# Optimization experiments

Measured on AMD Instinct MI355X. Metric: run time of the kernel, lower is better.

## Reference

```python
import jax, jax.numpy as jnp
import numpy as np

B, D, H, R, OUT = 16384, 1024, 4, 1024, 10
LN_EPS = 1e-5


def setup_inputs() -> dict:
    key = jax.random.key(0)
    ks = jax.random.split(key, 20)
    s_in = 1.0 / np.sqrt(D)
    s_hid = 1.0 / np.sqrt(H * R)
    inp = {
        'x': jax.random.normal(ks[0], (B, D), dtype=jnp.float32),
        # block 1
        'wr1': jax.random.normal(ks[1], (H, R, D), dtype=jnp.float32) * s_in,
        'br1': jnp.zeros((H, R), dtype=jnp.float32),
        'wl1': jax.random.normal(ks[2], (H, R, D), dtype=jnp.float32) * s_in,
        'bl1': jnp.zeros((H, R), dtype=jnp.float32),
        'we1': jax.random.normal(ks[3], (D, H * R), dtype=jnp.float32) * s_hid,
        'be1': jnp.zeros((D,), dtype=jnp.float32),
        'g1': jnp.ones((D,), dtype=jnp.float32),
        'b1': jnp.zeros((D,), dtype=jnp.float32),
        # block 2
        'wr2': jax.random.normal(ks[4], (H, R, D), dtype=jnp.float32) * s_in,
        'br2': jnp.zeros((H, R), dtype=jnp.float32),
        'wl2': jax.random.normal(ks[5], (H, R, D), dtype=jnp.float32) * s_in,
        'bl2': jnp.zeros((H, R), dtype=jnp.float32),
        'we2': jax.random.normal(ks[6], (D, H * R), dtype=jnp.float32) * s_hid,
        'be2': jnp.zeros((D,), dtype=jnp.float32),
        'g2': jnp.ones((D,), dtype=jnp.float32),
        'b2': jnp.zeros((D,), dtype=jnp.float32),
        # final linear
        'wf': jax.random.normal(ks[7], (OUT, D), dtype=jnp.float32) * s_in,
        'bf': jnp.zeros((OUT,), dtype=jnp.float32),
    }
    return inp


def _bilinear_block(x, wr, br, wl, bl, we, be):
    # per-basis right/left projections batched into one einsum each: [B,D] x [H,R,D] -> [B,H,R]
    right = jnp.einsum('bd,hrd->bhr', x, wr) + br
    left = jnp.einsum('bd,hrd->bhr', x, wl) + bl
    # elementwise bilinear interaction, concat bases along last dim -> [B, H*R]
    inter = (right * left).reshape(x.shape[0], -1)
    return inter @ we.T + be  # [B, D_out]


def _layernorm(x, g, b):
    mu = jnp.mean(x, axis=-1, keepdims=True)
    var = jnp.mean(jnp.square(x - mu), axis=-1, keepdims=True)
    return (x - mu) * jax.lax.rsqrt(var + LN_EPS) * g + b


def reference(x, wr1, br1, wl1, bl1, we1, be1, g1, b1,
              wr2, br2, wl2, bl2, we2, be2, g2, b2, wf, bf):
    # block 1: bilinear + residual + layernorm
    h = _layernorm(x + _bilinear_block(x, wr1, br1, wl1, bl1, we1, be1), g1, b1)
    # block 2
    h = _layernorm(h + _bilinear_block(h, wr2, br2, wl2, bl2, we2, be2), g2, b2)
    # final linear head
    return h @ wf.T + bf
```

## Files before the change

### kernel.cpp

```cpp
#include <hip/hip_runtime.h>
#include <hip/hip_fp16.h>

#define DEV static __device__ __forceinline__

typedef _Float16 f16;
typedef _Float16 f16x8 __attribute__((ext_vector_type(8)));
typedef _Float16 f16x4 __attribute__((ext_vector_type(4)));
typedef float f32x4 __attribute__((ext_vector_type(4)));

constexpr int BATCH = 16384;
constexpr int D = 1024;
constexpr int HR = 4096;
constexpr int NOUT = 10;

__global__ void k_conv4(const float* __restrict__ s0, f16* __restrict__ d0, int n0,
                        const float* __restrict__ s1, f16* __restrict__ d1, int n1,
                        const float* __restrict__ s2, f16* __restrict__ d2, int n2,
                        const float* __restrict__ s3, f16* __restrict__ d3, int n3) {
    int i = blockIdx.x * blockDim.x + threadIdx.x;
    const int st = gridDim.x * blockDim.x;
    const int tot = n0 + n1 + n2 + n3;
    for (; i < tot; i += st) {
        const float* s; f16* d; int j = i;
        if (j < n0) { s = s0; d = d0; }
        else {
            j -= n0;
            if (j < n1) { s = s1; d = d1; }
            else {
                j -= n1;
                if (j < n2) { s = s2; d = d2; }
                else { j -= n2; s = s3; d = d3; }
            }
        }
        float4 v = reinterpret_cast<const float4*>(s)[j];
        f16x4 h;
        h[0] = (f16)v.x; h[1] = (f16)v.y; h[2] = (f16)v.z; h[3] = (f16)v.w;
        reinterpret_cast<f16x4*>(d)[j] = h;
    }
}

DEV void stage16(void* lds, const void* g) {
    __builtin_amdgcn_global_load_lds(
        (const __attribute__((address_space(1))) void*)g,
        (__attribute__((address_space(3))) void*)lds,
        16, 0, 0);
}

DEV void xcd_map(int bid, int MT, int& mt, int& nt) {
    const int x = bid & 7, q = bid >> 3;
    const int mpx = MT >> 3;
    nt = q / mpx;
    mt = x * mpx + (q % mpx);
}

#define VMCNT(n) asm volatile("s_waitcnt vmcnt(" #n ")" ::: "memory")
#define BAR()    __builtin_amdgcn_s_barrier()
#define PRIO(p)  __builtin_amdgcn_s_setprio(p)

__global__ __launch_bounds__(512, 2) void k_gemm_dual(
    const f16* __restrict__ Xh, const f16* __restrict__ Wr, const f16* __restrict__ Wl,
    const float* __restrict__ br, const float* __restrict__ bl,
    f16* __restrict__ inter, int MT)
{
    extern __shared__ __align__(16) char smem[];
    constexpr int NT = 16;
    constexpr int BUF = 65536;
    constexpr int OA = 0, OR = 32768, OL = 49152;

    int mt, nt;
    xcd_map(blockIdx.x, MT, mt, nt);
    const int m0 = mt * 256, n0 = nt * 128;
    const int tid = threadIdx.x;
    const int lane = tid & 63, wid = tid >> 6;
    const int wm = wid >> 2, wn = wid & 3;
    const int fr = lane & 15, fq = lane >> 4;
    const int xs = (fr & 7) << 4;
    const int dst = tid * 16;

    const int lr = tid >> 3;
    const int cb = ((tid & 7) << 4) ^ ((lr & 7) << 4);
    const char* pA0 = (const char*)Xh + (size_t)(m0 + lr)       * 2048 + cb;
    const char* pA1 = (const char*)Xh + (size_t)(m0 + 128 + lr) * 2048 + cb;
    const char* pA2 = (const char*)Xh + (size_t)(m0 + 64 + lr)  * 2048 + cb;
    const char* pA3 = (const char*)Xh + (size_t)(m0 + 192 + lr) * 2048 + cb;
    const char* pR0 = (const char*)Wr + (size_t)(n0 + lr)       * 2048 + cb;
    const char* pR1 = (const char*)Wr + (size_t)(n0 + 64 + lr)  * 2048 + cb;
    const char* pL0 = (const char*)Wl + (size_t)(n0 + lr)       * 2048 + cb;
    const char* pL1 = (const char*)Wl + (size_t)(n0 + 64 + lr)  * 2048 + cb;

#define D_AOFF(mi,mf,ks) (OA + ((mi)*128 + wm*64 + (mf)*16 + fr)*128 + ((((ks)*64) + fq*16) ^ xs))
#define D_ROFF(nf,ks)    (OR + (wn*32 + (nf)*16 + fr)*128 + ((((ks)*64) + fq*16) ^ xs))
#define D_LOFF(nf,ks)    (OL + (wn*32 + (nf)*16 + fr)*128 + ((((ks)*64) + fq*16) ^ xs))

    f16x8 a[4][2], bR[2][2], bL[2][2];
    f32x4 accR[8][2] = {};
    f32x4 accL[8][2] = {};

    stage16(smem + OA + dst, pA0);          stage16(smem + OA + 8192 + dst, pA1);
    stage16(smem + OR + dst, pR0);          stage16(smem + OR + 8192 + dst, pR1);
    stage16(smem + OL + dst, pL0);          stage16(smem + OL + 8192 + dst, pL1);
    stage16(smem + OA + 16384 + dst, pA2);  stage16(smem + OA + 24576 + dst, pA3);
    VMCNT(4);
    BAR();

    long ko = 128;
    for (int t = 0; t < NT; ++t) {
        char* base = smem + (t & 1) * BUF;
        char* nb   = smem + ((t & 1) ^ 1) * BUF;
        const bool pf = (t + 1) < NT;

#pragma unroll
        for (int mf = 0; mf < 4; ++mf)
#pragma unroll
            for (int ks = 0; ks < 2; ++ks)
                a[mf][ks] = *(const f16x8*)(base + D_AOFF(0, mf, ks));
#pragma unroll
        for (int nf = 0; nf < 2; ++nf)
#pragma unroll
            for (int ks = 0; ks < 2; ++ks)
                bR[nf][ks] = *(const f16x8*)(base + D_ROFF(nf, ks));
        if (pf) { stage16(nb + OA + dst, pA0 + ko); stage16(nb + OA + 8192 + dst, pA1 + ko); }
        PRIO(1);
#pragma unroll
        for (int mf = 0; mf < 4; ++mf)
#pragma unroll
            for (int nf = 0; nf < 2; ++nf)
#pragma unroll
                for (int ks = 0; ks < 2; ++ks)
                    accR[mf][nf] = __builtin_amdgcn_mfma_f32_16x16x32_f16(a[mf][ks], bR[nf][ks], accR[mf][nf], 0, 0, 0);
        PRIO(0);
        if (pf) { VMCNT(4); } else { VMCNT(2); }
        BAR();

#pragma unroll
        for (int nf = 0; nf < 2; ++nf)
#pragma unroll
            for (int ks = 0; ks < 2; ++ks)
                bL[nf][ks] = *(const f16x8*)(base + D_LOFF(nf, ks));
        if (pf) { stage16(nb + OR + dst, pR0 + ko); stage16(nb + OR + 8192 + dst, pR1 + ko); }
        PRIO(1);
#pragma unroll
        for (int mf = 0; mf < 4; ++mf)
#pragma unroll
            for (int nf = 0; nf < 2; ++nf)
#pragma unroll
                for (int ks = 0; ks < 2; ++ks)
                    accL[mf][nf] = __builtin_amdgcn_mfma_f32_16x16x32_f16(a[mf][ks], bL[nf][ks], accL[mf][nf], 0, 0, 0);
        PRIO(0);
        if (pf) { VMCNT(4); } else { VMCNT(0); }
        BAR();

#pragma unroll
        for (int mf = 0; mf < 4; ++mf)
#pragma unroll
            for (int ks = 0; ks < 2; ++ks)
                a[mf][ks] = *(const f16x8*)(base + D_AOFF(1, mf, ks));
        if (pf) { stage16(nb + OL + dst, pL0 + ko); stage16(nb + OL + 8192 + dst, pL1 + ko); }
        PRIO(1);
#pragma unroll
        for (int mf = 0; mf < 4; ++mf)
#pragma unroll
            for (int nf = 0; nf < 2; ++nf)
#pragma unroll
                for (int ks = 0; ks < 2; ++ks)
                    accR[4 + mf][nf] = __builtin_amdgcn_mfma_f32_16x16x32_f16(a[mf][ks], bR[nf][ks], accR[4 + mf][nf], 0, 0, 0);
        PRIO(0);
        BAR();

        if (pf) { stage16(nb + OA + 16384 + dst, pA2 + ko); stage16(nb + OA + 24576 + dst, pA3 + ko); }
        PRIO(1);
#pragma unroll
        for (int mf = 0; mf < 4; ++mf)
#pragma unroll
            for (int nf = 0; nf < 2; ++nf)
#pragma unroll
                for (int ks = 0; ks < 2; ++ks)
                    accL[4 + mf][nf] = __builtin_amdgcn_mfma_f32_16x16x32_f16(a[mf][ks], bL[nf][ks], accL[4 + mf][nf], 0, 0, 0);
        PRIO(0);
        if (pf) { VMCNT(4); }
        BAR();

        ko += 128;
    }

#pragma unroll
    for (int nf = 0; nf < 2; ++nf) {
        const int gc = n0 + wn * 32 + nf * 16 + fr;
        const float brv = br[gc], blv = bl[gc];
#pragma unroll
        for (int mi = 0; mi < 2; ++mi)
#pragma unroll
            for (int mf = 0; mf < 4; ++mf) {
                const int gr0 = m0 + wm * 128 + mi * 64 + mf * 16 + fq * 4;
#pragma unroll
                for (int j = 0; j < 4; ++j) {
                    const float rv = accR[mi * 4 + mf][nf][j] + brv;
                    const float lv = accL[mi * 4 + mf][nf][j] + blv;
                    inter[(size_t)(gr0 + j) * HR + gc] = (f16)(rv * lv);
                }
            }
    }
#undef D_AOFF
#undef D_ROFF
#undef D_LOFF
}

__global__ __launch_bounds__(512, 2) void k_gemm_expand_f32r(
    const f16* __restrict__ Ain, const f16* __restrict__ Wt,
    const float* __restrict__ be, const float* __restrict__ resid,
    f16* __restrict__ E, int MT);
__global__ __launch_bounds__(512, 2) void k_gemm_expand_f16r(
    const f16* __restrict__ Ain, const f16* __restrict__ Wt,
    const float* __restrict__ be, const f16* __restrict__ resid,
    f16* __restrict__ E, int MT);

template <typename TR>
DEV void expand_body(const f16* Ain, const f16* Wt, const float* be,
                     const TR* resid, f16* E, int MT)
{
    extern __shared__ __align__(16) char smem[];
    constexpr int NT = 64;
    constexpr int BUF = 65536;
    constexpr int OA = 0, OB = 32768;

    int mt, nt;
    xcd_map(blockIdx.x, MT, mt, nt);
    const int m0 = mt * 256, n0 = nt * 256;
    const int tid = threadIdx.x;
    const int lane = tid & 63, wid = tid >> 6;
    const int wm = wid >> 2, wn = wid & 3;
    const int fr = lane & 15, fq = lane >> 4;
    const int xs = (fr & 7) << 4;
    const int dst = tid * 16;

    const int lr = tid >> 3;
    const int cb = ((tid & 7) << 4) ^ ((lr & 7) << 4);
    const char* pA0 = (const char*)Ain + (size_t)(m0 + lr)       * 8192 + cb;
    const char* pA1 = (const char*)Ain + (size_t)(m0 + 128 + lr) * 8192 + cb;
    const char* pA2 = (const char*)Ain + (size_t)(m0 + 64 + lr)  * 8192 + cb;
    const char* pA3 = (const char*)Ain + (size_t)(m0 + 192 + lr) * 8192 + cb;
    const int r5 = lr & 31, wn2 = lr >> 5;
    const char* pB0 = (const char*)Wt + (size_t)(n0 + wn2 * 64 + r5)        * 8192 + cb;
    const char* pB1 = (const char*)Wt + (size_t)(n0 + (2 + wn2) * 64 + r5)  * 8192 + cb;
    const char* pB2 = (const char*)Wt + (size_t)(n0 + wn2 * 64 + 32 + r5)       * 8192 + cb;
    const char* pB3 = (const char*)Wt + (size_t)(n0 + (2 + wn2) * 64 + 32 + r5) * 8192 + cb;

#define E_AOFF(mi,mf,ks) (OA + ((mi)*128 + wm*64 + (mf)*16 + fr)*128 + ((((ks)*64) + fq*16) ^ xs))
#define E_BOFF(ni,nf,ks) (OB + ((ni)*128 + wn*32 + (nf)*16 + fr)*128 + ((((ks)*64) + fq*16) ^ xs))

    f16x8 a[4][2], b0[2][2], b1[2][2];
    f32x4 acc[8][4] = {};

    stage16(smem + OA + dst, pA0);          stage16(smem + OA + 8192 + dst, pA1);
    stage16(smem + OB + dst, pB0);          stage16(smem + OB + 8192 + dst, pB1);
    stage16(smem + OB + 16384 + dst, pB2);  stage16(smem + OB + 24576 + dst, pB3);
    stage16(smem + OA + 16384 + dst, pA2);  stage16(smem + OA + 24576 + dst, pA3);
    VMCNT(4);
    BAR();

    long ko = 128;
    for (int t = 0; t < NT; ++t) {
        char* base = smem + (t & 1) * BUF;
        char* nb   = smem + ((t & 1) ^ 1) * BUF;
        const bool pf = (t + 1) < NT;

#pragma unroll
        for (int mf = 0; mf < 4; ++mf)
#pragma unroll
            for (int ks = 0; ks < 2; ++ks)
                a[mf][ks] = *(const f16x8*)(base + E_AOFF(0, mf, ks));
#pragma unroll
        for (int nf = 0; nf < 2; ++nf)
#pragma unroll
            for (int ks = 0; ks < 2; ++ks)
                b0[nf][ks] = *(const f16x8*)(base + E_BOFF(0, nf, ks));
        if (pf) { stage16(nb + OA + dst, pA0 + ko); stage16(nb + OA + 8192 + dst, pA1 + ko); }
        PRIO(1);
#pragma unroll
        for (int mf = 0; mf < 4; ++mf)
#pragma unroll
            for (int nf = 0; nf < 2; ++nf)
#pragma unroll
                for (int ks = 0; ks < 2; ++ks)
                    acc[mf][nf] = __builtin_amdgcn_mfma_f32_16x16x32_f16(a[mf][ks], b0[nf][ks], acc[mf][nf], 0, 0, 0);
        PRIO(0);
        if (pf) { VMCNT(4); } else { VMCNT(2); }
        BAR();

#pragma unroll
        for (int nf = 0; nf < 2; ++nf)
#pragma unroll
            for (int ks = 0; ks < 2; ++ks)
                b1[nf][ks] = *(const f16x8*)(base + E_BOFF(1, nf, ks));
        if (pf) { stage16(nb + OB + dst, pB0 + ko); stage16(nb + OB + 8192 + dst, pB1 + ko); }
        PRIO(1);
#pragma unroll
        for (int mf = 0; mf < 4; ++mf)
#pragma unroll
            for (int nf = 0; nf < 2; ++nf)
#pragma unroll
                for (int ks = 0; ks < 2; ++ks)
                    acc[mf][2 + nf] = __builtin_amdgcn_mfma_f32_16x16x32_f16(a[mf][ks], b1[nf][ks], acc[mf][2 + nf], 0, 0, 0);
        PRIO(0);
        if (pf) { VMCNT(4); } else { VMCNT(0); }
        BAR();

#pragma unroll
        for (int mf = 0; mf < 4; ++mf)
#pragma unroll
            for (int ks = 0; ks < 2; ++ks)
                a[mf][ks] = *(const f16x8*)(base + E_AOFF(1, mf, ks));
        if (pf) { stage16(nb + OB + 16384 + dst, pB2 + ko); stage16(nb + OB + 24576 + dst, pB3 + ko); }
        PRIO(1);
#pragma unroll
        for (int mf = 0; mf < 4; ++mf)
#pragma unroll
            for (int nf = 0; nf < 2; ++nf)
#pragma unroll
                for (int ks = 0; ks < 2; ++ks)
                    acc[4 + mf][nf] = __builtin_amdgcn_mfma_f32_16x16x32_f16(a[mf][ks], b0[nf][ks], acc[4 + mf][nf], 0, 0, 0);
        PRIO(0);
        BAR();

        if (pf) { stage16(nb + OA + 16384 + dst, pA2 + ko); stage16(nb + OA + 24576 + dst, pA3 + ko); }
        PRIO(1);
#pragma unroll
        for (int mf = 0; mf < 4; ++mf)
#pragma unroll
            for (int nf = 0; nf < 2; ++nf)
#pragma unroll
                for (int ks = 0; ks < 2; ++ks)
                    acc[4 + mf][2 + nf] = __builtin_amdgcn_mfma_f32_16x16x32_f16(a[mf][ks], b1[nf][ks], acc[4 + mf][2 + nf], 0, 0, 0);
        PRIO(0);
        if (pf) { VMCNT(4); }
        BAR();

        ko += 128;
    }

#pragma unroll
    for (int ni = 0; ni < 2; ++ni)
#pragma unroll
        for (int nf = 0; nf < 2; ++nf) {
            const int gc = n0 + wn * 64 + ni * 32 + nf * 16 + fr;
            const float bev = be[gc];
#pragma unroll
            for (int mi = 0; mi < 2; ++mi)
#pragma unroll
                for (int mf = 0; mf < 4; ++mf) {
                    const int gr0 = m0 + wm * 128 + mi * 64 + mf * 16 + fq * 4;
#pragma unroll
                    for (int j = 0; j < 4; ++j) {
                        const float rv = (float)resid[(size_t)(gr0 + j) * D + gc];
                        E[(size_t)(gr0 + j) * D + gc] = (f16)(acc[mi * 4 + mf][ni * 2 + nf][j] + bev + rv);
                    }
                }
        }
#undef E_AOFF
#undef E_BOFF
}

__global__ __launch_bounds__(512, 2) void k_gemm_expand_f32r(
    const f16* __restrict__ Ain, const f16* __restrict__ Wt,
    const float* __restrict__ be, const float* __restrict__ resid,
    f16* __restrict__ E, int MT)
{ expand_body<float>(Ain, Wt, be, resid, E, MT); }

__global__ __launch_bounds__(512, 2) void k_gemm_expand_f16r(
    const f16* __restrict__ Ain, const f16* __restrict__ Wt,
    const float* __restrict__ be, const f16* __restrict__ resid,
    f16* __restrict__ E, int MT)
{ expand_body<f16>(Ain, Wt, be, resid, E, MT); }

__global__ __launch_bounds__(256) void k_ln(
    f16* __restrict__ EH, const float* __restrict__ g, const float* __restrict__ bb)
{
    const int wid = threadIdx.x >> 6, lane = threadIdx.x & 63;
    const int row = blockIdx.x * 4 + wid;
    f16* er = EH + (size_t)row * D;
    float v[16];
    float s = 0.f, sq = 0.f;
#pragma unroll
    for (int k = 0; k < 16; ++k) {
        const int c = lane + 64 * k;
        v[k] = (float)er[c];
        s += v[k];
        sq += v[k] * v[k];
    }
#pragma unroll
    for (int off = 32; off; off >>= 1) {
        s += __shfl_down(s, off);
        sq += __shfl_down(sq, off);
    }
    s = __shfl(s, 0);
    sq = __shfl(sq, 0);
    const float mu = s * (1.0f / D);
    const float var = sq * (1.0f / D) - mu * mu;
    const float rs = rsqrtf(var + 1e-5f);
#pragma unroll
    for (int k = 0; k < 16; ++k) {
        const int c = lane + 64 * k;
        const float o = (v[k] - mu) * rs * g[c] + bb[c];
        er[c] = (f16)o;
    }
}

__global__ __launch_bounds__(256) void k_head(
    const f16* __restrict__ Hf, const float* __restrict__ Wf,
    const float* __restrict__ bf, float* __restrict__ outp)
{
    __shared__ float wfs[NOUT * D];
    for (int i = threadIdx.x; i < NOUT * D; i += 256) wfs[i] = Wf[i];
    __syncthreads();
    const int wid = threadIdx.x >> 6, lane = threadIdx.x & 63;
    const int row = blockIdx.x * 4 + wid;
    const f16* hr = Hf + (size_t)row * D;
    float hv[16];
#pragma unroll
    for (int k = 0; k < 16; ++k) hv[k] = (float)hr[lane + 64 * k];
#pragma unroll
    for (int j = 0; j < NOUT; ++j) {
        float p = 0.f;
#pragma unroll
        for (int k = 0; k < 16; ++k) p += hv[k] * wfs[j * D + lane + 64 * k];
#pragma unroll
        for (int off = 32; off; off >>= 1) p += __shfl_down(p, off);
        if (lane == 0) outp[(size_t)row * NOUT + j] = p + bf[j];
    }
}

extern "C" void kernel_launch(void* const* d_in, const int* in_sizes, int n_in,
                              void* d_out, int out_size, void* d_ws, size_t ws_size,
                              hipStream_t stream) {
    (void)in_sizes; (void)n_in; (void)out_size;
    const float* x   = (const float*)d_in[0];
    const float* wr1 = (const float*)d_in[1];
    const float* br1 = (const float*)d_in[2];
    const float* wl1 = (const float*)d_in[3];
    const float* bl1 = (const float*)d_in[4];
    const float* we1 = (const float*)d_in[5];
    const float* be1 = (const float*)d_in[6];
    const float* g1  = (const float*)d_in[7];
    const float* b1  = (const float*)d_in[8];
    const float* wr2 = (const float*)d_in[9];
    const float* br2 = (const float*)d_in[10];
    const float* wl2 = (const float*)d_in[11];
    const float* bl2 = (const float*)d_in[12];
    const float* we2 = (const float*)d_in[13];
    const float* be2 = (const float*)d_in[14];
    const float* g2  = (const float*)d_in[15];
    const float* b2  = (const float*)d_in[16];
    const float* wf  = (const float*)d_in[17];
    const float* bf  = (const float*)d_in[18];
    float* outp = (float*)d_out;

    constexpr size_t SZ_W16 = (size_t)HR * D * sizeof(f16);
    constexpr size_t SZ_A16 = (size_t)BATCH * D * sizeof(f16);
    constexpr int SMEM = 2 * 65536;

    hipFuncSetAttribute((const void*)k_gemm_dual,        hipFuncAttributeMaxDynamicSharedMemorySize, SMEM);
    hipFuncSetAttribute((const void*)k_gemm_expand_f32r, hipFuncAttributeMaxDynamicSharedMemorySize, SMEM);
    hipFuncSetAttribute((const void*)k_gemm_expand_f16r, hipFuncAttributeMaxDynamicSharedMemorySize, SMEM);

    char* p = (char*)d_ws;
    f16* wrh = (f16*)p; p += SZ_W16;
    f16* wlh = (f16*)p; p += SZ_W16;
    f16* weh = (f16*)p; p += SZ_W16;
    f16* xh  = (f16*)p; p += SZ_A16;
    f16* EH  = (f16*)p; p += SZ_A16;
    f16* interh = (f16*)p;
    const size_t base = (size_t)(p - (char*)d_ws);
    const size_t avail = ws_size > base ? ws_size - base : 0;

    int CH = 2048;
    if ((size_t)16384 * HR * sizeof(f16) <= avail) CH = 16384;
    else if ((size_t)8192 * HR * sizeof(f16) <= avail) CH = 8192;
    else if ((size_t)4096 * HR * sizeof(f16) <= avail) CH = 4096;

    const int nch = BATCH / CH;
    const int MT = CH / 256;
    const int gDual = MT * (HR / 128);
    const int gExp  = MT * (D / 256);

    constexpr int NW4 = HR * D / 4;
    k_conv4<<<2048, 256, 0, stream>>>(x, xh, BATCH * D / 4,
                                      wr1, wrh, NW4, wl1, wlh, NW4, we1, weh, NW4);

    for (int c = 0; c < nch; ++c) {
        k_gemm_dual<<<gDual, 512, SMEM, stream>>>(xh + (size_t)c * CH * D, wrh, wlh, br1, bl1, interh, MT);
        k_gemm_expand_f32r<<<gExp, 512, SMEM, stream>>>(interh, weh, be1, x + (size_t)c * CH * D,
                                                        EH + (size_t)c * CH * D, MT);
    }
    k_ln<<<BATCH / 4, 256, 0, stream>>>(EH, g1, b1);

    k_conv4<<<1536, 256, 0, stream>>>(wr2, wrh, NW4, wl2, wlh, NW4, we2, weh, NW4,
                                      nullptr, nullptr, 0);

    for (int c = 0; c < nch; ++c) {
        k_gemm_dual<<<gDual, 512, SMEM, stream>>>(EH + (size_t)c * CH * D, wrh, wlh, br2, bl2, interh, MT);
        k_gemm_expand_f16r<<<gExp, 512, SMEM, stream>>>(interh, weh, be2, EH + (size_t)c * CH * D,
                                                        EH + (size_t)c * CH * D, MT);
    }
    k_ln<<<BATCH / 4, 256, 0, stream>>>(EH, g2, b2);

    k_head<<<BATCH / 4, 256, 0, stream>>>(EH, wf, bf, outp);
}
```

Baseline: 803.6 us.

## Restructure GEMM mainloops with triple-buffered weights and one barrier per k-step

In both the dual projection GEMM and the expand GEMM, the shared-memory plan changes. The activation tile stays double-buffered, while the weight tiles are now triple-buffered and prefetched two k-steps ahead. Each k-iteration now runs all MFMAs for both halves with a single barrier and vmcnt wait, instead of four barrier-separated phases. The aim is to cut barrier stalls and hide global-load latency better. In exchange, dynamic LDS per block grows to 160 KB, which fills the whole LDS, and register pressure may rise because both operand sets stay live across the longer compute phase.

```diff
diff --git a/kernel.cpp b/kernel.cpp
--- a/kernel.cpp
+++ b/kernel.cpp
@@ -64,8 +64,8 @@
 {
     extern __shared__ __align__(16) char smem[];
     constexpr int NT = 16;
-    constexpr int BUF = 65536;
-    constexpr int OA = 0, OR = 32768, OL = 49152;
+    constexpr int BUFA = 32768, BUFR = 16384;
+    constexpr int OR = 65536, OL = 65536 + 3 * BUFR;
 
     int mt, nt;
     xcd_map(blockIdx.x, MT, mt, nt);
@@ -88,99 +88,91 @@
     const char* pL0 = (const char*)Wl + (size_t)(n0 + lr)       * 2048 + cb;
     const char* pL1 = (const char*)Wl + (size_t)(n0 + 64 + lr)  * 2048 + cb;
 
-#define D_AOFF(mi,mf,ks) (OA + ((mi)*128 + wm*64 + (mf)*16 + fr)*128 + ((((ks)*64) + fq*16) ^ xs))
-#define D_ROFF(nf,ks)    (OR + (wn*32 + (nf)*16 + fr)*128 + ((((ks)*64) + fq*16) ^ xs))
-#define D_LOFF(nf,ks)    (OL + (wn*32 + (nf)*16 + fr)*128 + ((((ks)*64) + fq*16) ^ xs))
+#define D_AOFF(mi,mf,ks) (((mi)*128 + wm*64 + (mf)*16 + fr)*128 + ((((ks)*64) + fq*16) ^ xs))
+#define D_BOFF(nf,ks)    ((wn*32 + (nf)*16 + fr)*128 + ((((ks)*64) + fq*16) ^ xs))
 
     f16x8 a[4][2], bR[2][2], bL[2][2];
     f32x4 accR[8][2] = {};
     f32x4 accL[8][2] = {};
 
-    stage16(smem + OA + dst, pA0);          stage16(smem + OA + 8192 + dst, pA1);
+    stage16(smem + dst, pA0);               stage16(smem + 8192 + dst, pA1);
+    stage16(smem + 16384 + dst, pA2);       stage16(smem + 24576 + dst, pA3);
     stage16(smem + OR + dst, pR0);          stage16(smem + OR + 8192 + dst, pR1);
     stage16(smem + OL + dst, pL0);          stage16(smem + OL + 8192 + dst, pL1);
-    stage16(smem + OA + 16384 + dst, pA2);  stage16(smem + OA + 24576 + dst, pA3);
+    stage16(smem + OR + BUFR + dst, pR0 + 128);  stage16(smem + OR + BUFR + 8192 + dst, pR1 + 128);
+    stage16(smem + OL + BUFR + dst, pL0 + 128);  stage16(smem + OL + BUFR + 8192 + dst, pL1 + 128);
     VMCNT(4);
     BAR();
 
-    long ko = 128;
+    int aPar = 0, r3 = 0;
+    long ko = 128, ko2 = 256;
     for (int t = 0; t < NT; ++t) {
-        char* base = smem + (t & 1) * BUF;
-        char* nb   = smem + ((t & 1) ^ 1) * BUF;
-        const bool pf = (t + 1) < NT;
+        char* Ab = smem + aPar * BUFA;
+        char* Rb = smem + OR + r3 * BUFR;
+        char* Lb = smem + OL + r3 * BUFR;
+        const bool pf1 = (t + 1) < NT;
+        const bool pf2 = (t + 2) < NT;
+        const int r3n = (r3 == 0) ? 2 : r3 - 1;
 
 #pragma unroll
         for (int mf = 0; mf < 4; ++mf)
 #pragma unroll
             for (int ks = 0; ks < 2; ++ks)
-                a[mf][ks] = *(const f16x8*)(base + D_AOFF(0, mf, ks));
+                a[mf][ks] = *(const f16x8*)(Ab + D_AOFF(0, mf, ks));
 #pragma unroll
         for (int nf = 0; nf < 2; ++nf)
 #pragma unroll
+            for (int ks = 0; ks < 2; ++ks) {
+                bR[nf][ks] = *(const f16x8*)(Rb + D_BOFF(nf, ks));
+                bL[nf][ks] = *(const f16x8*)(Lb + D_BOFF(nf, ks));
+            }
+        if (pf1) {
+            char* nA = smem + (aPar ^ 1) * BUFA;
+            stage16(nA + dst, pA0 + ko);          stage16(nA + 8192 + dst, pA1 + ko);
+            stage16(nA + 16384 + dst, pA2 + ko);  stage16(nA + 24576 + dst, pA3 + ko);
+        }
+        if (pf2) {
+            char* nR = smem + OR + r3n * BUFR;
+            char* nL = smem + OL + r3n * BUFR;
+            stage16(nR + dst, pR0 + ko2);  stage16(nR + 8192 + dst, pR1 + ko2);
+            stage16(nL + dst, pL0 + ko2);  stage16(nL + 8192 + dst, pL1 + ko2);
+        }
+        PRIO(1);
+#pragma unroll
+        for (int mf = 0; mf < 4; ++mf)
+#pragma unroll
+            for (int nf = 0; nf < 2; ++nf)
+#pragma unroll
+                for (int ks = 0; ks < 2; ++ks) {
+                    accR[mf][nf] = __builtin_amdgcn_mfma_f32_16x16x32_f16(a[mf][ks], bR[nf][ks], accR[mf][nf], 0, 0, 0);
+                    accL[mf][nf] = __builtin_amdgcn_mfma_f32_16x16x32_f16(a[mf][ks], bL[nf][ks], accL[mf][nf], 0, 0, 0);
+                }
+        PRIO(0);
+
+#pragma unroll
+        for (int mf = 0; mf < 4; ++mf)
+#pragma unroll
             for (int ks = 0; ks < 2; ++ks)
-                bR[nf][ks] = *(const f16x8*)(base + D_ROFF(nf, ks));
-        if (pf) { stage16(nb + OA + dst, pA0 + ko); stage16(nb + OA + 8192 + dst, pA1 + ko); }
+                a[mf][ks] = *(const f16x8*)(Ab + D_AOFF(1, mf, ks));
         PRIO(1);
 #pragma unroll
         for (int mf = 0; mf < 4; ++mf)
 #pragma unroll
             for (int nf = 0; nf < 2; ++nf)
 #pragma unroll
-                for (int ks = 0; ks < 2; ++ks)
-                    accR[mf][nf] = __builtin_amdgcn_mfma_f32_16x16x32_f16(a[mf][ks], bR[nf][ks], accR[mf][nf], 0, 0, 0);
+                for (int ks = 0; ks < 2; ++ks) {
+                    accR[4 + mf][nf] = __builtin_amdgcn_mfma_f32_16x16x32_f16(a[mf][ks], bR[nf][ks], accR[4 + mf][nf], 0, 0, 0);
+                    accL[4 + mf][nf] = __builtin_amdgcn_mfma_f32_16x16x32_f16(a[mf][ks], bL[nf][ks], accL[4 + mf][nf], 0, 0, 0);
+                }
         PRIO(0);
-        if (pf) { VMCNT(4); } else { VMCNT(2); }
+
+        if (pf2) { VMCNT(4); } else if (pf1) { VMCNT(0); }
         BAR();
 
-#pragma unroll
-        for (int nf = 0; nf < 2; ++nf)
-#pragma unroll
-            for (int ks = 0; ks < 2; ++ks)
-                bL[nf][ks] = *(const f16x8*)(base + D_LOFF(nf, ks));
-        if (pf) { stage16(nb + OR + dst, pR0 + ko); stage16(nb + OR + 8192 + dst, pR1 + ko); }
-        PRIO(1);
-#pragma unroll
-        for (int mf = 0; mf < 4; ++mf)
-#pragma unroll
-            for (int nf = 0; nf < 2; ++nf)
-#pragma unroll
-                for (int ks = 0; ks < 2; ++ks)
-                    accL[mf][nf] = __builtin_amdgcn_mfma_f32_16x16x32_f16(a[mf][ks], bL[nf][ks], accL[mf][nf], 0, 0, 0);
-        PRIO(0);
-        if (pf) { VMCNT(4); } else { VMCNT(0); }
-        BAR();
-
-#pragma unroll
-        for (int mf = 0; mf < 4; ++mf)
-#pragma unroll
-            for (int ks = 0; ks < 2; ++ks)
-                a[mf][ks] = *(const f16x8*)(base + D_AOFF(1, mf, ks));
-        if (pf) { stage16(nb + OL + dst, pL0 + ko); stage16(nb + OL + 8192 + dst, pL1 + ko); }
-        PRIO(1);
-#pragma unroll
-        for (int mf = 0; mf < 4; ++mf)
-#pragma unroll
-            for (int nf = 0; nf < 2; ++nf)
-#pragma unroll
-                for (int ks = 0; ks < 2; ++ks)
-                    accR[4 + mf][nf] = __builtin_amdgcn_mfma_f32_16x16x32_f16(a[mf][ks], bR[nf][ks], accR[4 + mf][nf], 0, 0, 0);
-        PRIO(0);
-        BAR();
-
-        if (pf) { stage16(nb + OA + 16384 + dst, pA2 + ko); stage16(nb + OA + 24576 + dst, pA3 + ko); }
-        PRIO(1);
-#pragma unroll
-        for (int mf = 0; mf < 4; ++mf)
-#pragma unroll
-            for (int nf = 0; nf < 2; ++nf)
-#pragma unroll
-                for (int ks = 0; ks < 2; ++ks)
-                    accL[4 + mf][nf] = __builtin_amdgcn_mfma_f32_16x16x32_f16(a[mf][ks], bL[nf][ks], accL[4 + mf][nf], 0, 0, 0);
-        PRIO(0);
-        if (pf) { VMCNT(4); }
-        BAR();
-
+        aPar ^= 1;
+        r3 = (r3 == 2) ? 0 : r3 + 1;
         ko += 128;
+        ko2 += 128;
     }
 
 #pragma unroll
@@ -201,18 +193,8 @@
             }
     }
 #undef D_AOFF
-#undef D_ROFF
-#undef D_LOFF
-}
-
-__global__ __launch_bounds__(512, 2) void k_gemm_expand_f32r(
-    const f16* __restrict__ Ain, const f16* __restrict__ Wt,
-    const float* __restrict__ be, const float* __restrict__ resid,
-    f16* __restrict__ E, int MT);
-__global__ __launch_bounds__(512, 2) void k_gemm_expand_f16r(
-    const f16* __restrict__ Ain, const f16* __restrict__ Wt,
-    const float* __restrict__ be, const f16* __restrict__ resid,
-    f16* __restrict__ E, int MT);
+#undef D_BOFF
+}
 
 template <typename TR>
 DEV void expand_body(const f16* Ain, const f16* Wt, const float* be,
@@ -220,8 +202,8 @@
 {
     extern __shared__ __align__(16) char smem[];
     constexpr int NT = 64;
-    constexpr int BUF = 65536;
-    constexpr int OA = 0, OB = 32768;
+    constexpr int BUFA = 32768, BUFB = 32768;
+    constexpr int OB = 65536;
 
     int mt, nt;
     xcd_map(blockIdx.x, MT, mt, nt);
@@ -245,97 +227,88 @@
     const char* pB2 = (const char*)Wt + (size_t)(n0 + wn2 * 64 + 32 + r5)       * 8192 + cb;
     const char* pB3 = (const char*)Wt + (size_t)(n0 + (2 + wn2) * 64 + 32 + r5) * 8192 + cb;
 
-#define E_AOFF(mi,mf,ks) (OA + ((mi)*128 + wm*64 + (mf)*16 + fr)*128 + ((((ks)*64) + fq*16) ^ xs))
-#define E_BOFF(ni,nf,ks) (OB + ((ni)*128 + wn*32 + (nf)*16 + fr)*128 + ((((ks)*64) + fq*16) ^ xs))
+#define E_AOFF(mi,mf,ks) (((mi)*128 + wm*64 + (mf)*16 + fr)*128 + ((((ks)*64) + fq*16) ^ xs))
+#define E_BOFF(ni,nf,ks) (((ni)*128 + wn*32 + (nf)*16 + fr)*128 + ((((ks)*64) + fq*16) ^ xs))
 
     f16x8 a[4][2], b0[2][2], b1[2][2];
     f32x4 acc[8][4] = {};
 
-    stage16(smem + OA + dst, pA0);          stage16(smem + OA + 8192 + dst, pA1);
+    stage16(smem + dst, pA0);               stage16(smem + 8192 + dst, pA1);
+    stage16(smem + 16384 + dst, pA2);       stage16(smem + 24576 + dst, pA3);
     stage16(smem + OB + dst, pB0);          stage16(smem + OB + 8192 + dst, pB1);
     stage16(smem + OB + 16384 + dst, pB2);  stage16(smem + OB + 24576 + dst, pB3);
-    stage16(smem + OA + 16384 + dst, pA2);  stage16(smem + OA + 24576 + dst, pA3);
+    stage16(smem + OB + BUFB + dst, pB0 + 128);          stage16(smem + OB + BUFB + 8192 + dst, pB1 + 128);
+    stage16(smem + OB + BUFB + 16384 + dst, pB2 + 128);  stage16(smem + OB + BUFB + 24576 + dst, pB3 + 128);
     VMCNT(4);
     BAR();
 
-    long ko = 128;
+    int aPar = 0, b3 = 0;
+    long ko = 128, ko2 = 256;
     for (int t = 0; t < NT; ++t) {
-        char* base = smem + (t & 1) * BUF;
-        char* nb   = smem + ((t & 1) ^ 1) * BUF;
-        const bool pf = (t + 1) < NT;
+        char* Ab = smem + aPar * BUFA;
+        char* Bb = smem + OB + b3 * BUFB;
+        const bool pf1 = (t + 1) < NT;
+        const bool pf2 = (t + 2) < NT;
+        const int b3n = (b3 == 0) ? 2 : b3 - 1;
 
 #pragma unroll
         for (int mf = 0; mf < 4; ++mf)
 #pragma unroll
             for (int ks = 0; ks < 2; ++ks)
-                a[mf][ks] = *(const f16x8*)(base + E_AOFF(0, mf, ks));
+                a[mf][ks] = *(const f16x8*)(Ab + E_AOFF(0, mf, ks));
 #pragma unroll
         for (int nf = 0; nf < 2; ++nf)
 #pragma unroll
+            for (int ks = 0; ks < 2; ++ks) {
+                b0[nf][ks] = *(const f16x8*)(Bb + E_BOFF(0, nf, ks));
+                b1[nf][ks] = *(const f16x8*)(Bb + E_BOFF(1, nf, ks));
+            }
+        if (pf1) {
+            char* nA = smem + (aPar ^ 1) * BUFA;
+            stage16(nA + dst, pA0 + ko);          stage16(nA + 8192 + dst, pA1 + ko);
+            stage16(nA + 16384 + dst, pA2 + ko);  stage16(nA + 24576 + dst, pA3 + ko);
+        }
+        if (pf2) {
+            char* nB = smem + OB + b3n * BUFB;
+            stage16(nB + dst, pB0 + ko2);          stage16(nB + 8192 + dst, pB1 + ko2);
+            stage16(nB + 16384 + dst, pB2 + ko2);  stage16(nB + 24576 + dst, pB3 + ko2);
+        }
+        PRIO(1);
+#pragma unroll
+        for (int mf = 0; mf < 4; ++mf)
+#pragma unroll
+            for (int nf = 0; nf < 2; ++nf)
+#pragma unroll
+                for (int ks = 0; ks < 2; ++ks) {
+                    acc[mf][nf]     = __builtin_amdgcn_mfma_f32_16x16x32_f16(a[mf][ks], b0[nf][ks], acc[mf][nf], 0, 0, 0);
+                    acc[mf][2 + nf] = __builtin_amdgcn_mfma_f32_16x16x32_f16(a[mf][ks], b1[nf][ks], acc[mf][2 + nf], 0, 0, 0);
+                }
+        PRIO(0);
+
+#pragma unroll
+        for (int mf = 0; mf < 4; ++mf)
+#pragma unroll
             for (int ks = 0; ks < 2; ++ks)
-                b0[nf][ks] = *(const f16x8*)(base + E_BOFF(0, nf, ks));
-        if (pf) { stage16(nb + OA + dst, pA0 + ko); stage16(nb + OA + 8192 + dst, pA1 + ko); }
+                a[mf][ks] = *(const f16x8*)(Ab + E_AOFF(1, mf, ks));
         PRIO(1);
 #pragma unroll
         for (int mf = 0; mf < 4; ++mf)
 #pragma unroll
             for (int nf = 0; nf < 2; ++nf)
 #pragma unroll
-                for (int ks = 0; ks < 2; ++ks)
-                    acc[mf][nf] = __builtin_amdgcn_mfma_f32_16x16x32_f16(a[mf][ks], b0[nf][ks], acc[mf][nf], 0, 0, 0);
+                for (int ks = 0; ks < 2; ++ks) {
+                    acc[4 + mf][nf]     = __builtin_amdgcn_mfma_f32_16x16x32_f16(a[mf][ks], b0[nf][ks], acc[4 + mf][nf], 0, 0, 0);
+                    acc[4 + mf][2 + nf] = __builtin_amdgcn_mfma_f32_16x16x32_f16(a[mf][ks], b1[nf][ks], acc[4 + mf][2 + nf], 0, 0, 0);
+                }
         PRIO(0);
-        if (pf) { VMCNT(4); } else { VMCNT(2); }
+
+        if (pf2) { VMCNT(4); } else if (pf1) { VMCNT(0); }
         BAR();
 
-#pragma unroll
-        for (int nf = 0; nf < 2; ++nf)
-#pragma unroll
-            for (int ks = 0; ks < 2; ++ks)
-                b1[nf][ks] = *(const f16x8*)(base + E_BOFF(1, nf, ks));
-        if (pf) { stage16(nb + OB + dst, pB0 + ko); stage16(nb + OB + 8192 + dst, pB1 + ko); }
-        PRIO(1);
-#pragma unroll
-        for (int mf = 0; mf < 4; ++mf)
-#pragma unroll
-            for (int nf = 0; nf < 2; ++nf)
-#pragma unroll
-                for (int ks = 0; ks < 2; ++ks)
-                    acc[mf][2 + nf] = __builtin_amdgcn_mfma_f32_16x16x32_f16(a[mf][ks], b1[nf][ks], acc[mf][2 + nf], 0, 0, 0);
-        PRIO(0);
-        if (pf) { VMCNT(4); } else { VMCNT(0); }
-        BAR();
-
-#pragma unroll
-        for (int mf = 0; mf < 4; ++mf)
-#pragma unroll
-            for (int ks = 0; ks < 2; ++ks)
-                a[mf][ks] = *(const f16x8*)(base + E_AOFF(1, mf, ks));
-        if (pf) { stage16(nb + OB + 16384 + dst, pB2 + ko); stage16(nb + OB + 24576 + dst, pB3 + ko); }
-        PRIO(1);
-#pragma unroll
-        for (int mf = 0; mf < 4; ++mf)
-#pragma unroll
-            for (int nf = 0; nf < 2; ++nf)
-#pragma unroll
-                for (int ks = 0; ks < 2; ++ks)
-                    acc[4 + mf][nf] = __builtin_amdgcn_mfma_f32_16x16x32_f16(a[mf][ks], b0[nf][ks], acc[4 + mf][nf], 0, 0, 0);
-        PRIO(0);
-        BAR();
-
-        if (pf) { stage16(nb + OA + 16384 + dst, pA2 + ko); stage16(nb + OA + 24576 + dst, pA3 + ko); }
-        PRIO(1);
-#pragma unroll
-        for (int mf = 0; mf < 4; ++mf)
-#pragma unroll
-            for (int nf = 0; nf < 2; ++nf)
-#pragma unroll
-                for (int ks = 0; ks < 2; ++ks)
-                    acc[4 + mf][2 + nf] = __builtin_amdgcn_mfma_f32_16x16x32_f16(a[mf][ks], b1[nf][ks], acc[4 + mf][2 + nf], 0, 0, 0);
-        PRIO(0);
-        if (pf) { VMCNT(4); }
-        BAR();
-
+        aPar ^= 1;
+        b3 = (b3 == 2) ? 0 : b3 + 1;
         ko += 128;
+        ko2 += 128;
     }
 
 #pragma unroll
@@ -456,7 +429,7 @@
 
     constexpr size_t SZ_W16 = (size_t)HR * D * sizeof(f16);
     constexpr size_t SZ_A16 = (size_t)BATCH * D * sizeof(f16);
-    constexpr int SMEM = 2 * 65536;
+    constexpr int SMEM = 163840;
 
     hipFuncSetAttribute((const void*)k_gemm_dual,        hipFuncAttributeMaxDynamicSharedMemorySize, SMEM);
     hipFuncSetAttribute((const void*)k_gemm_expand_f32r, hipFuncAttributeMaxDynamicSharedMemorySize, SMEM);
```

New measurement: 819.5 us. About the same (+2.0%).
